# Kernel tuning notes

Hardware: AMD Instinct MI355X
Metric: run time of the kernel (lower is better)

Reference implementation:

```python
import jax, jax.numpy as jnp
import numpy as np

D_MODEL = 1024
NUM_HEADS = 16
D_K = D_MODEL // NUM_HEADS
B, S = 2, 2048


def setup_inputs() -> dict:
    key = jax.random.key(0)
    ks = jax.random.split(key, 9)
    scale = 1.0 / np.sqrt(D_MODEL)
    return {
        "hidden_states": jax.random.normal(ks[0], (B, S, D_MODEL), dtype=jnp.float32),
        "attention_mask": jnp.ones((B, S, S), dtype=jnp.int32),
        "Wq": jax.random.normal(ks[1], (D_MODEL, D_MODEL), dtype=jnp.float32) * scale,
        "bq": jnp.zeros((D_MODEL,), dtype=jnp.float32),
        "Wk": jax.random.normal(ks[2], (D_MODEL, D_MODEL), dtype=jnp.float32) * scale,
        "bk": jnp.zeros((D_MODEL,), dtype=jnp.float32),
        "Wv": jax.random.normal(ks[3], (D_MODEL, D_MODEL), dtype=jnp.float32) * scale,
        "bv": jnp.zeros((D_MODEL,), dtype=jnp.float32),
        "Wo": jax.random.normal(ks[4], (D_MODEL, D_MODEL), dtype=jnp.float32) * scale,
        "bo": jnp.zeros((D_MODEL,), dtype=jnp.float32),
    }


def reference(hidden_states, attention_mask, Wq, bq, Wk, bk, Wv, bv, Wo, bo):
    b, s, _ = hidden_states.shape
    # torch Linear: y = x @ W.T + b
    def proj(W, bias):
        y = jnp.einsum('bsd,ed->bse', hidden_states, W) + bias
        return y.reshape(b, s, NUM_HEADS, D_K).transpose(0, 2, 1, 3)  # [B,H,S,dk]
    q = proj(Wq, bq)
    k = proj(Wk, bk)
    v = proj(Wv, bv)
    scores = jnp.einsum('bnqd,bnkd->bnqk', q, k) / np.sqrt(D_K)
    mask = attention_mask[:, None, :, :]  # [B,1,S,S]
    scores = jnp.where(mask == 0, jnp.float32(-1e9), scores)
    attn = jax.nn.softmax(scores, axis=-1)  # dropout = identity (eval)
    ctx = jnp.einsum('bnqk,bnkd->bnqd', attn, v)
    ctx = ctx.transpose(0, 2, 1, 3).reshape(b, s, D_MODEL)
    return jnp.einsum('bsd,ed->bse', ctx, Wo) + bo
```

## Files before the change

kernel.cpp:

```cpp
#include <hip/hip_runtime.h>

typedef short short8 __attribute__((ext_vector_type(8)));
typedef float floatx4 __attribute__((ext_vector_type(4)));
typedef float floatx16 __attribute__((ext_vector_type(16)));
typedef unsigned short ushort4v __attribute__((ext_vector_type(4)));

#define DEV static __device__ __forceinline__

DEV unsigned short f2bf(float f) {
  unsigned int u = __builtin_bit_cast(unsigned int, f);
  u += 0x7fffu + ((u >> 16) & 1u);
  return (unsigned short)(u >> 16);
}

DEV unsigned int pkbf2(float a, float b) {
  unsigned int ua = __builtin_bit_cast(unsigned int, a) + 0x8000u;
  unsigned int ub = __builtin_bit_cast(unsigned int, b) + 0x8000u;
  return (ua >> 16) | (ub & 0xffff0000u);
}

DEV void gload16(const unsigned short* g, unsigned short* l) {
  __builtin_amdgcn_global_load_lds((__attribute__((address_space(1))) void*)g,
                                   (__attribute__((address_space(3))) void*)l,
                                   16, 0, 0);
}

__global__ void convert_kernel(const float* __restrict__ hs, const float* __restrict__ Wq,
                               const float* __restrict__ Wk, const float* __restrict__ Wv,
                               const float* __restrict__ Wo,
                               unsigned short* __restrict__ xbf, unsigned short* __restrict__ wqkv,
                               unsigned short* __restrict__ wobf) {
  size_t i4 = ((size_t)blockIdx.x * 256 + threadIdx.x) * 4;
  const float* src;
  unsigned short* dst;
  if (i4 < 4194304) {
    src = hs + i4; dst = xbf + i4;
  } else if (i4 < 7340032) {
    size_t o = i4 - 4194304;
    size_t lo = o & 1048575;
    src = (o < 1048576) ? (Wq + lo) : ((o < 2097152) ? (Wk + lo) : (Wv + lo));
    dst = wqkv + o;
  } else {
    size_t o = i4 - 7340032;
    src = Wo + o; dst = wobf + o;
  }
  float4 v = *(const float4*)src;
  ushort4v u;
  u.x = f2bf(v.x); u.y = f2bf(v.y); u.z = f2bf(v.z); u.w = f2bf(v.w);
  *(ushort4v*)dst = u;
}

__global__ void maskpack_kernel(const int* __restrict__ mask, unsigned long long* __restrict__ bits) {
  int w = blockIdx.x * 256 + threadIdx.x;
  const int4* p = (const int4*)(mask + (size_t)w * 64);
  unsigned long long r = 0ull;
#pragma unroll
  for (int j = 0; j < 16; ++j) {
    int4 m = p[j];
    r |= (unsigned long long)(m.x != 0) << (j * 4 + 0);
    r |= (unsigned long long)(m.y != 0) << (j * 4 + 1);
    r |= (unsigned long long)(m.z != 0) << (j * 4 + 2);
    r |= (unsigned long long)(m.w != 0) << (j * 4 + 3);
  }
  bits[w] = r;
}

__global__ void __launch_bounds__(256) qkv_gemm(
    const unsigned short* __restrict__ X, const unsigned short* __restrict__ W,
    const float* __restrict__ bq, const float* __restrict__ bk, const float* __restrict__ bv,
    unsigned short* __restrict__ Qb, unsigned short* __restrict__ Kb,
    unsigned short* __restrict__ Vt) {
  __shared__ __align__(16) unsigned short As[128 * 32];
  __shared__ __align__(16) unsigned short Bs[128 * 32];
  const int tid = threadIdx.x;
  const int lane = tid & 63, wv = tid >> 6;
  const int wm = wv >> 1, wn = wv & 1;
  const int quad = lane >> 4, l15 = lane & 15;
  const int mb = blockIdx.y, nb = blockIdx.x;
  const bool sw = (nb < 16);

  const unsigned short* ga = X + (size_t)(mb * 128 + (tid >> 2)) * 1024 + (tid & 3) * 8;
  const unsigned short* gb = W + (size_t)(nb * 128 + (tid >> 2)) * 1024 + (tid & 3) * 8;
  unsigned short* la1 = As + tid * 8;
  unsigned short* la2 = As + 2048 + tid * 8;
  unsigned short* lb1 = Bs + tid * 8;
  unsigned short* lb2 = Bs + 2048 + tid * 8;

  const int wx = sw ? wn : wm;
  const int ww = sw ? wm : wn;

  floatx4 acc[4][4] = {};
  for (int kt = 0; kt < 32; ++kt) {
    const int k0 = kt * 32;
    gload16(ga + k0, la1);
    gload16(ga + k0 + 65536, la2);
    gload16(gb + k0, lb1);
    gload16(gb + k0 + 65536, lb2);
    __syncthreads();
    short8 xa[4], wb[4];
#pragma unroll
    for (int i = 0; i < 4; ++i) {
      xa[i] = *(const short8*)&As[(wx * 64 + i * 16 + l15) * 32 + quad * 8];
      wb[i] = *(const short8*)&Bs[(ww * 64 + i * 16 + l15) * 32 + quad * 8];
    }
    if (sw) {
#pragma unroll
      for (int mt = 0; mt < 4; ++mt)
#pragma unroll
        for (int nt = 0; nt < 4; ++nt)
          acc[mt][nt] = __builtin_amdgcn_mfma_f32_16x16x32_bf16(wb[mt], xa[nt], acc[mt][nt], 0, 0, 0);
    } else {
#pragma unroll
      for (int mt = 0; mt < 4; ++mt)
#pragma unroll
        for (int nt = 0; nt < 4; ++nt)
          acc[mt][nt] = __builtin_amdgcn_mfma_f32_16x16x32_bf16(xa[mt], wb[nt], acc[mt][nt], 0, 0, 0);
    }
    __syncthreads();
  }

  if (sw) {
#pragma unroll
    for (int mt = 0; mt < 4; ++mt) {
      const int wc0 = nb * 128 + wm * 64 + mt * 16 + quad * 4;
      const int mat = wc0 >> 10;
      const int nl0 = wc0 & 1023;
      const int hh = nl0 >> 6, d0 = nl0 & 63;
      const float4 b4 = *(const float4*)((mat ? bk : bq) + nl0);
      unsigned short* dst = mat ? Kb : Qb;
#pragma unroll
      for (int nt = 0; nt < 4; ++nt) {
        const int colx = mb * 128 + wn * 64 + nt * 16 + l15;
        const int bb = colx >> 11, s = colx & 2047;
        ushort4v pv;
        pv[0] = f2bf(acc[mt][nt][0] + b4.x);
        pv[1] = f2bf(acc[mt][nt][1] + b4.y);
        pv[2] = f2bf(acc[mt][nt][2] + b4.z);
        pv[3] = f2bf(acc[mt][nt][3] + b4.w);
        *(ushort4v*)&dst[((size_t)(bb * 16 + hh) * 2048 + s) * 64 + d0] = pv;
      }
    }
  } else {
#pragma unroll
    for (int nt = 0; nt < 4; ++nt) {
      const int col = nb * 128 + wn * 64 + nt * 16 + l15;
      const int nl = col & 1023;
      const float bias = bv[nl];
      const int hh = nl >> 6, d = nl & 63;
#pragma unroll
      for (int mt = 0; mt < 4; ++mt) {
        const int row0 = mb * 128 + wm * 64 + mt * 16 + quad * 4;
        const int bb = row0 >> 11, s = row0 & 2047;
        ushort4v pv;
#pragma unroll
        for (int r = 0; r < 4; ++r) pv[r] = f2bf(acc[mt][nt][r] + bias);
        *(ushort4v*)&Vt[((size_t)(bb * 16 + hh) * 64 + d) * 2048 + s] = pv;
      }
    }
  }
}

__global__ void __launch_bounds__(128, 2) attn_kernel(
    const unsigned short* __restrict__ Qb, const unsigned short* __restrict__ Kb,
    const unsigned short* __restrict__ Vt, const unsigned long long* __restrict__ mbits,
    unsigned short* __restrict__ ctx) {
  __shared__ __align__(16) unsigned short Ks[128 * 64];
  __shared__ __align__(16) unsigned short Vs[64 * 128];
  const int tid = threadIdx.x;
  const int lane = tid & 63, wv = tid >> 6;
  const int l31 = lane & 31, h = lane >> 5;
  const int pair = blockIdx.x >> 5, qt = blockIdx.x & 31;
  const int b_ = pair >> 4, hd = pair & 15;
  const int qg = qt * 64 + wv * 32 + l31;
  const size_t pbase = (size_t)pair * (2048 * 64);

  short8 qf[4];
#pragma unroll
  for (int ks = 0; ks < 4; ++ks)
    qf[ks] = *(const short8*)(Qb + pbase + (size_t)qg * 64 + ks * 16 + h * 8);

  floatx16 acc_o[2] = {};
  float lsum = 0.f;
  const float SCL = 0.125f * 1.44269504088896340736f;
  const float NC = -10.0f;

  for (int kb16 = 0; kb16 < 16; ++kb16) {
    __syncthreads();
#pragma unroll
    for (int it = 0; it < 8; ++it) {
      const int row = it * 16 + (tid >> 3);
      const int c = tid & 7;
      short8 v = *(const short8*)(Kb + pbase + (size_t)(kb16 * 128 + row) * 64 + c * 8);
      *(short8*)&Ks[row * 64 + ((c ^ (row & 7)) * 8)] = v;
    }
#pragma unroll
    for (int it = 0; it < 8; ++it) {
      const int row = it * 8 + (tid >> 4);
      const int c = tid & 15;
      short8 v = *(const short8*)(Vt + (size_t)pair * (64 * 2048) + (size_t)row * 2048 + kb16 * 128 + c * 8);
      *(short8*)&Vs[row * 128 + ((c ^ ((row & 7) << 1)) * 8)] = v;
    }
    __syncthreads();

    const unsigned long long* mrow = mbits + ((size_t)b_ * 2048 + qg) * 32 + kb16 * 2;
    const unsigned long long w0 = mrow[0], w1 = mrow[1];

    floatx16 accs[4] = {};
#pragma unroll
    for (int ks = 0; ks < 4; ++ks)
#pragma unroll
      for (int kb = 0; kb < 4; ++kb) {
        const int krow = kb * 32 + l31;
        short8 kf = *(const short8*)&Ks[krow * 64 + (((ks * 2 + h) ^ (krow & 7)) * 8)];
        accs[kb] = __builtin_amdgcn_mfma_f32_32x32x16_bf16(kf, qf[ks], accs[kb], 0, 0, 0);
      }

    if (__any((w0 & w1) != ~0ull)) {
#pragma unroll
      for (int kb = 0; kb < 4; ++kb) {
        const unsigned long long w = (kb < 2) ? w0 : w1;
#pragma unroll
        for (int reg = 0; reg < 16; ++reg) {
          const int kl = (reg & 3) + 8 * (reg >> 2) + 4 * h;
          const int bit = (kb & 1) * 32 + kl;
          if (!((w >> bit) & 1ull)) accs[kb][reg] = -6e9f;
        }
      }
    }

#pragma unroll
    for (int kb = 0; kb < 4; ++kb) {
      unsigned int pk[8];
#pragma unroll
      for (int i = 0; i < 8; ++i) {
        const float a = exp2f(fmaf(accs[kb][2 * i], SCL, NC));
        const float b = exp2f(fmaf(accs[kb][2 * i + 1], SCL, NC));
        lsum += a + b;
        pk[i] = pkbf2(a, b);
      }
#pragma unroll
      for (int u = 0; u < 2; ++u) {
        const unsigned int own0 = h ? pk[4 * u + 2] : pk[4 * u + 0];
        const unsigned int own1 = h ? pk[4 * u + 3] : pk[4 * u + 1];
        const unsigned int snd0 = h ? pk[4 * u + 0] : pk[4 * u + 2];
        const unsigned int snd1 = h ? pk[4 * u + 1] : pk[4 * u + 3];
        const unsigned int t0 = __shfl_xor(snd0, 32);
        const unsigned int t1 = __shfl_xor(snd1, 32);
        union { unsigned int w[4]; short8 s8; } af;
        af.w[0] = h ? t0 : own0;
        af.w[1] = h ? t1 : own1;
        af.w[2] = h ? own0 : t0;
        af.w[3] = h ? own1 : t1;
        const int t = kb * 2 + u;
#pragma unroll
        for (int nt = 0; nt < 2; ++nt) {
          const int vrow = nt * 32 + l31;
          short8 vf = *(const short8*)&Vs[vrow * 128 + (((t * 2 + h) ^ ((vrow & 7) << 1)) * 8)];
          acc_o[nt] = __builtin_amdgcn_mfma_f32_32x32x16_bf16(af.s8, vf, acc_o[nt], 0, 0, 0);
        }
      }
    }
  }

  lsum += __shfl_xor(lsum, 32);
  const float rinv = 1.f / ((lsum > 0.f) ? lsum : 1.f);

#pragma unroll
  for (int reg = 0; reg < 16; ++reg) {
    const int ql = (reg & 3) + 8 * (reg >> 2) + 4 * h;
    const float rl = __shfl(rinv, ql);
    const size_t base = ((size_t)b_ * 2048 + qt * 64 + wv * 32 + ql) * 1024 + hd * 64;
    ctx[base + l31]      = f2bf(acc_o[0][reg] * rl);
    ctx[base + 32 + l31] = f2bf(acc_o[1][reg] * rl);
  }
}

__global__ void __launch_bounds__(256) out_gemm(
    const unsigned short* __restrict__ C, const unsigned short* __restrict__ W,
    const float* __restrict__ bo, float* __restrict__ out) {
  __shared__ __align__(16) unsigned short As[128 * 32];
  __shared__ __align__(16) unsigned short Bs[128 * 32];
  const int tid = threadIdx.x;
  const int lane = tid & 63, wv = tid >> 6;
  const int wm = wv >> 1, wn = wv & 1;
  const int quad = lane >> 4, l15 = lane & 15;
  const int mb = blockIdx.y, nb = blockIdx.x;

  const unsigned short* ga = C + (size_t)(mb * 128 + (tid >> 2)) * 1024 + (tid & 3) * 8;
  const unsigned short* gb = W + (size_t)(nb * 128 + (tid >> 2)) * 1024 + (tid & 3) * 8;
  unsigned short* la1 = As + tid * 8;
  unsigned short* la2 = As + 2048 + tid * 8;
  unsigned short* lb1 = Bs + tid * 8;
  unsigned short* lb2 = Bs + 2048 + tid * 8;

  floatx4 acc[4][4] = {};
  for (int kt = 0; kt < 32; ++kt) {
    const int k0 = kt * 32;
    gload16(ga + k0, la1);
    gload16(ga + k0 + 65536, la2);
    gload16(gb + k0, lb1);
    gload16(gb + k0 + 65536, lb2);
    __syncthreads();
    short8 af[4], bfr[4];
#pragma unroll
    for (int i = 0; i < 4; ++i) {
      af[i]  = *(const short8*)&As[(wm * 64 + i * 16 + l15) * 32 + quad * 8];
      bfr[i] = *(const short8*)&Bs[(wn * 64 + i * 16 + l15) * 32 + quad * 8];
    }
#pragma unroll
    for (int mt = 0; mt < 4; ++mt)
#pragma unroll
      for (int nt = 0; nt < 4; ++nt)
        acc[mt][nt] = __builtin_amdgcn_mfma_f32_16x16x32_bf16(af[mt], bfr[nt], acc[mt][nt], 0, 0, 0);
    __syncthreads();
  }
#pragma unroll
  for (int nt = 0; nt < 4; ++nt) {
    const int col = nb * 128 + wn * 64 + nt * 16 + l15;
    const float bias = bo[col];
#pragma unroll
    for (int mt = 0; mt < 4; ++mt)
#pragma unroll
      for (int r = 0; r < 4; ++r) {
        const int row = mb * 128 + wm * 64 + mt * 16 + quad * 4 + r;
        out[(size_t)row * 1024 + col] = acc[mt][nt][r] + bias;
      }
  }
}

extern "C" void kernel_launch(void* const* d_in, const int* in_sizes, int n_in,
                              void* d_out, int out_size, void* d_ws, size_t ws_size,
                              hipStream_t stream) {
  const float* hs = (const float*)d_in[0];
  const int* mask = (const int*)d_in[1];
  const float* Wq = (const float*)d_in[2];
  const float* bq = (const float*)d_in[3];
  const float* Wk = (const float*)d_in[4];
  const float* bk = (const float*)d_in[5];
  const float* Wv = (const float*)d_in[6];
  const float* bv = (const float*)d_in[7];
  const float* Wo = (const float*)d_in[8];
  const float* bo = (const float*)d_in[9];
  float* out = (float*)d_out;

  char* ws = (char*)d_ws;
  unsigned short* xbf  = (unsigned short*)(ws + 0);
  unsigned short* wqkv = (unsigned short*)(ws + 8388608);
  unsigned short* wobf = (unsigned short*)(ws + 14680064);
  unsigned short* Qb   = (unsigned short*)(ws + 16777216);
  unsigned short* Kb   = (unsigned short*)(ws + 25165824);
  unsigned short* Vt   = (unsigned short*)(ws + 33554432);
  unsigned short* ctx  = (unsigned short*)(ws + 41943040);
  unsigned long long* mbits = (unsigned long long*)(ws + 50331648);

  convert_kernel<<<8192, 256, 0, stream>>>(hs, Wq, Wk, Wv, Wo, xbf, wqkv, wobf);
  maskpack_kernel<<<512, 256, 0, stream>>>(mask, mbits);
  qkv_gemm<<<dim3(24, 32), 256, 0, stream>>>(xbf, wqkv, bq, bk, bv, Qb, Kb, Vt);
  attn_kernel<<<1024, 128, 0, stream>>>(Qb, Kb, Vt, mbits, ctx);
  out_gemm<<<dim3(8, 32), 256, 0, stream>>>(ctx, wobf, bo, out);
}
```

Baseline: 262.6 us.

## Prefetch next K/V tile into registers and use permlane32 swap in attention

The attention loop now loads the next 128-key K and V tiles and mask words into registers while the current tile is computed, then stores them to LDS at the top of the next iteration. This overlaps global memory latency with MFMA work. The change also replaces the pair of shfl_xor exchanges with permlane32_swap, raises wave priority around the MFMA blocks, and splits the row-sum into four accumulators. The register prefetch adds about 64 VGPRs per thread, which may lower occupancy.

Result: slower. 312.5 us (+19.0%).

```diff
diff --git a/kernel.cpp b/kernel.cpp
--- a/kernel.cpp
+++ b/kernel.cpp
@@ -179,33 +179,47 @@
   for (int ks = 0; ks < 4; ++ks)
     qf[ks] = *(const short8*)(Qb + pbase + (size_t)qg * 64 + ks * 16 + h * 8);
 
+  const unsigned short* kg = Kb + pbase + (size_t)(tid >> 3) * 64 + (tid & 7) * 8;
+  const unsigned short* vg = Vt + (size_t)pair * (size_t)(64 * 2048) + (size_t)(tid >> 4) * 2048 + (tid & 15) * 8;
+  unsigned short* klp = Ks + (tid >> 3) * 64 + (((tid & 7) ^ ((tid >> 3) & 7)) * 8);
+  unsigned short* vlp = Vs + (tid >> 4) * 128 + (((tid & 15) ^ (((tid >> 4) & 7) << 1)) * 8);
+
+  const unsigned long long* mrow = mbits + ((size_t)b_ * 2048 + qg) * 32;
+
+  short8 kreg[8], vreg[8];
+#pragma unroll
+  for (int it = 0; it < 8; ++it) kreg[it] = *(const short8*)(kg + it * 1024);
+#pragma unroll
+  for (int it = 0; it < 8; ++it) vreg[it] = *(const short8*)(vg + it * 16384);
+  unsigned long long w0 = mrow[0], w1 = mrow[1];
+
   floatx16 acc_o[2] = {};
-  float lsum = 0.f;
+  float lacc[4] = {0.f, 0.f, 0.f, 0.f};
   const float SCL = 0.125f * 1.44269504088896340736f;
   const float NC = -10.0f;
 
   for (int kb16 = 0; kb16 < 16; ++kb16) {
     __syncthreads();
 #pragma unroll
-    for (int it = 0; it < 8; ++it) {
-      const int row = it * 16 + (tid >> 3);
-      const int c = tid & 7;
-      short8 v = *(const short8*)(Kb + pbase + (size_t)(kb16 * 128 + row) * 64 + c * 8);
-      *(short8*)&Ks[row * 64 + ((c ^ (row & 7)) * 8)] = v;
-    }
-#pragma unroll
-    for (int it = 0; it < 8; ++it) {
-      const int row = it * 8 + (tid >> 4);
-      const int c = tid & 15;
-      short8 v = *(const short8*)(Vt + (size_t)pair * (64 * 2048) + (size_t)row * 2048 + kb16 * 128 + c * 8);
-      *(short8*)&Vs[row * 128 + ((c ^ ((row & 7) << 1)) * 8)] = v;
-    }
-    __syncthreads();
-
-    const unsigned long long* mrow = mbits + ((size_t)b_ * 2048 + qg) * 32 + kb16 * 2;
-    const unsigned long long w0 = mrow[0], w1 = mrow[1];
+    for (int it = 0; it < 8; ++it) *(short8*)(klp + it * 1024) = kreg[it];
+#pragma unroll
+    for (int it = 0; it < 8; ++it) *(short8*)(vlp + it * 1024) = vreg[it];
+    __syncthreads();
+
+    unsigned long long nw0 = 0ull, nw1 = 0ull;
+    if (kb16 < 15) {
+      const size_t ko = (size_t)(kb16 + 1) * 8192;
+      const int vo = (kb16 + 1) * 128;
+#pragma unroll
+      for (int it = 0; it < 8; ++it) kreg[it] = *(const short8*)(kg + ko + it * 1024);
+#pragma unroll
+      for (int it = 0; it < 8; ++it) vreg[it] = *(const short8*)(vg + vo + it * 16384);
+      nw0 = mrow[kb16 * 2 + 2];
+      nw1 = mrow[kb16 * 2 + 3];
+    }
 
     floatx16 accs[4] = {};
+    __builtin_amdgcn_s_setprio(1);
 #pragma unroll
     for (int ks = 0; ks < 4; ++ks)
 #pragma unroll
@@ -214,6 +228,7 @@
         short8 kf = *(const short8*)&Ks[krow * 64 + (((ks * 2 + h) ^ (krow & 7)) * 8)];
         accs[kb] = __builtin_amdgcn_mfma_f32_32x32x16_bf16(kf, qf[ks], accs[kb], 0, 0, 0);
       }
+    __builtin_amdgcn_s_setprio(0);
 
     if (__any((w0 & w1) != ~0ull)) {
 #pragma unroll
@@ -231,37 +246,39 @@
 #pragma unroll
     for (int kb = 0; kb < 4; ++kb) {
       unsigned int pk[8];
+      float ls = 0.f;
 #pragma unroll
       for (int i = 0; i < 8; ++i) {
         const float a = exp2f(fmaf(accs[kb][2 * i], SCL, NC));
         const float b = exp2f(fmaf(accs[kb][2 * i + 1], SCL, NC));
-        lsum += a + b;
+        ls += a + b;
         pk[i] = pkbf2(a, b);
       }
+      lacc[kb] += ls;
 #pragma unroll
       for (int u = 0; u < 2; ++u) {
-        const unsigned int own0 = h ? pk[4 * u + 2] : pk[4 * u + 0];
-        const unsigned int own1 = h ? pk[4 * u + 3] : pk[4 * u + 1];
-        const unsigned int snd0 = h ? pk[4 * u + 0] : pk[4 * u + 2];
-        const unsigned int snd1 = h ? pk[4 * u + 1] : pk[4 * u + 3];
-        const unsigned int t0 = __shfl_xor(snd0, 32);
-        const unsigned int t1 = __shfl_xor(snd1, 32);
+        auto r02 = __builtin_amdgcn_permlane32_swap(pk[4 * u + 0], pk[4 * u + 2], false, false);
+        auto r13 = __builtin_amdgcn_permlane32_swap(pk[4 * u + 1], pk[4 * u + 3], false, false);
         union { unsigned int w[4]; short8 s8; } af;
-        af.w[0] = h ? t0 : own0;
-        af.w[1] = h ? t1 : own1;
-        af.w[2] = h ? own0 : t0;
-        af.w[3] = h ? own1 : t1;
+        af.w[0] = r02[0];
+        af.w[1] = r13[0];
+        af.w[2] = r02[1];
+        af.w[3] = r13[1];
         const int t = kb * 2 + u;
+        __builtin_amdgcn_s_setprio(1);
 #pragma unroll
         for (int nt = 0; nt < 2; ++nt) {
           const int vrow = nt * 32 + l31;
           short8 vf = *(const short8*)&Vs[vrow * 128 + (((t * 2 + h) ^ ((vrow & 7) << 1)) * 8)];
           acc_o[nt] = __builtin_amdgcn_mfma_f32_32x32x16_bf16(af.s8, vf, acc_o[nt], 0, 0, 0);
         }
-      }
-    }
-  }
-
+        __builtin_amdgcn_s_setprio(0);
+      }
+    }
+    w0 = nw0; w1 = nw1;
+  }
+
+  float lsum = (lacc[0] + lacc[1]) + (lacc[2] + lacc[3]);
   lsum += __shfl_xor(lsum, 32);
   const float rinv = 1.f / ((lsum > 0.f) ? lsum : 1.f);
 
```
